# Optimization experiments

Measured on AMD Instinct MI355X. Metric: run time of the kernel, lower is better.

## Reference

```python
import jax, jax.numpy as jnp
import numpy as np

TOP_K = 32
NUM_RBF = 16
D_MIN, D_MAX = 2.0, 22.0
MAX_REL = 32  # max_relative_feature

# atom index order: N=0, Ca=1, C=2, O=3, Cb=4
# 24 (query, neighbor) atom pairs, in the exact order of the torch RBF_all list
_PA = np.array([0,2,3,4,1,1,1,1,0,0,0,4,4,3,0,2,3,4,2,3,4,2,3,2])
_PB = np.array([0,2,3,4,0,2,3,4,2,3,4,2,3,2,1,1,1,1,0,0,0,4,4,3])


def setup_inputs() -> dict:
    key = jax.random.key(0)
    ks = jax.random.split(key, 6)
    B, L = 4, 2048
    X = jax.random.normal(ks[0], (B, L, 4, 3), jnp.float32) * 3.0  # coords, ~protein scale
    mask = jnp.ones((B, L), jnp.float32)
    residue_idx = jnp.tile(jnp.arange(L, dtype=jnp.int32)[None, :], (B, 1))
    chain_labels = jax.random.randint(ks[1], (B, L), 0, 4)
    W_pos = jax.random.normal(ks[2], (2 * MAX_REL + 2, 16), jnp.float32) * 0.1  # [66,16]
    b_pos = jnp.zeros((16,), jnp.float32)
    W_edge = jax.random.normal(ks[3], (16 + 25 * NUM_RBF, 128), jnp.float32) * 0.05  # [416,128]
    ln_gamma = jnp.ones((128,), jnp.float32)
    ln_beta = jnp.zeros((128,), jnp.float32)
    return dict(X=X, mask=mask, residue_idx=residue_idx, chain_labels=chain_labels,
                W_pos=W_pos, b_pos=b_pos, W_edge=W_edge, ln_gamma=ln_gamma, ln_beta=ln_beta)


def _rbf(D):
    mu = jnp.linspace(D_MIN, D_MAX, NUM_RBF)
    sigma = (D_MAX - D_MIN) / NUM_RBF
    return jnp.exp(-(((D[..., None] - mu) / sigma) ** 2))


def reference(X, mask, residue_idx, chain_labels, W_pos, b_pos, W_edge, ln_gamma, ln_beta):
    B, L = X.shape[0], X.shape[1]
    N, Ca, C, O = X[:, :, 0], X[:, :, 1], X[:, :, 2], X[:, :, 3]
    b = Ca - N
    c = C - Ca
    a = jnp.cross(b, c)
    Cb = -0.58273431 * a + 0.56802827 * b - 0.54067466 * c + Ca

    # kNN graph on Ca distances (masked)
    m2 = mask[:, None, :] * mask[:, :, None]                      # [B,L,L]
    dX = Ca[:, None, :, :] - Ca[:, :, None, :]
    D = m2 * jnp.sqrt(jnp.sum(dX * dX, -1) + 1e-6)                # [B,L,L]
    D_max = jnp.max(D, -1, keepdims=True)
    D_adjust = D + (1.0 - m2) * D_max
    neg_vals, E_idx = jax.lax.top_k(-D_adjust, TOP_K)             # smallest-k
    D_neighbors = -neg_vals                                       # [B,L,K]

    atoms = jnp.stack([N, Ca, C, O, Cb], 0)                       # [5,B,L,3]
    bidx = jnp.arange(B)[:, None, None]
    nbr = atoms[:, bidx, E_idx]                                   # [5,B,L,K,3] gathered neighbor coords

    # 24 cross-atom RBFs (gather-then-distance == distance-then-gather)
    Aq = atoms[_PA]                                               # [24,B,L,3]
    Nk = nbr[_PB]                                                 # [24,B,L,K,3]
    Dp = jnp.sqrt(jnp.sum((Aq[:, :, :, None, :] - Nk) ** 2, -1) + 1e-6)  # [24,B,L,K]
    R0 = _rbf(D_neighbors)                                        # [B,L,K,16] (Ca-Ca)
    Rp = jnp.moveaxis(_rbf(Dp), 0, 3).reshape(B, L, TOP_K, 24 * NUM_RBF)
    RBF_all = jnp.concatenate([R0, Rp], -1)                       # [B,L,K,400]

    # positional / chain encodings
    ridx_nbr = residue_idx[bidx, E_idx]                           # [B,L,K]
    offset = residue_idx[:, :, None] - ridx_nbr
    ch_nbr = chain_labels[bidx, E_idx]
    E_chains = (chain_labels[:, :, None] == ch_nbr).astype(jnp.int32)
    d = jnp.clip(offset + MAX_REL, 0, 2 * MAX_REL) * E_chains + (1 - E_chains) * (2 * MAX_REL + 1)
    E_pos = W_pos[d] + b_pos                                      # one-hot @ W == row gather

    E = jnp.concatenate([E_pos, RBF_all], -1) @ W_edge            # [B,L,K,128]
    mu = E.mean(-1, keepdims=True)
    var = E.var(-1, keepdims=True)
    E = (E - mu) / jnp.sqrt(var + 1e-5) * ln_gamma + ln_beta
    return E, E_idx
```

## Files before the change

kernel.cpp:

```cpp
#include <hip/hip_runtime.h>
#include <stdint.h>

typedef _Float16 v8h __attribute__((ext_vector_type(8)));
typedef _Float16 v4h __attribute__((ext_vector_type(4)));
typedef float v4f __attribute__((ext_vector_type(4)));

#define BB 4
#define LL 2048
#define TOPK 32
#define NF 416
#define NOUT 128
#define NBINS 4096
#define NCAND 128
#define FBS 72

__device__ __constant__ int c_PA[24] = {0,2,3,4,1,1,1,1,0,0,0,4,4,3,0,2,3,4,2,3,4,2,3,2};
__device__ __constant__ int c_PB[24] = {0,2,3,4,0,2,3,4,2,3,4,2,3,2,1,1,1,1,0,0,0,4,4,3};

#define OFF_ATOMS 0u
#define OFF_CA    524288u
#define OFF_WT    655360u

#define HPERM(x) ((((x) & 15) << 8) | ((x) >> 4))

static __device__ inline int tk_bin(unsigned u) {
  int v = (int)(u >> 17) - 8000;
  v = v < 0 ? 0 : v;
  return v > 4095 ? 4095 : v;
}

static __device__ inline float dist_np(float4 a, float4 b) {
#pragma clang fp contract(off)
  float dx = a.x - b.x, dy = a.y - b.y, dz = a.z - b.z;
  float s = ((dx * dx + dy * dy) + dz * dz) + 1e-6f;
  return sqrtf(s);
}

static __device__ inline unsigned long long umin64(unsigned long long a, unsigned long long b) {
  return a < b ? a : b;
}
static __device__ inline unsigned long long umax64(unsigned long long a, unsigned long long b) {
  return a > b ? a : b;
}

static __device__ inline void rbf16w(float d, _Float16* dst) {
  v8h z = {};
  *(v8h*)dst = z;
  *(v8h*)(dst + 8) = z;
  float m0f = ceilf((d - 7.204f) * 0.75f);
  m0f = fmaxf(0.0f, fminf(8.0f, m0f));
  const float C  = 0.96089780f;
  const float SC = 1.28119707f;
  float a0 = d * C - 1.92179560f - m0f * SC;
  _Float16* p = dst + (int)m0f;
#pragma unroll
  for (int t = 0; t < 8; ++t) {
    float a = a0 - (float)t * SC;
    float v = __builtin_amdgcn_exp2f(-(a * a));
    p[t] = (_Float16)v;
  }
}

static __device__ inline float pdist(const float* qa, const float* nb, int pp) {
  int ia = c_PA[pp] * 3, ib = c_PB[pp] * 3;
  float dx = qa[ia] - nb[ib];
  float dy = qa[ia + 1] - nb[ib + 1];
  float dz = qa[ia + 2] - nb[ib + 2];
  return sqrtf(dx * dx + dy * dy + dz * dz + 1e-6f);
}

__global__ __launch_bounds__(256) void prep_kernel(const float* __restrict__ X,
                                                   const float* __restrict__ W_edge,
                                                   float4* __restrict__ atomsP,
                                                   float4* __restrict__ CaP,
                                                   _Float16* __restrict__ Wt) {
  int idx = blockIdx.x * 256 + threadIdx.x;
  if (idx < BB * LL) {
    const float* xp = X + (size_t)idx * 12;
    float Nx = xp[0], Ny = xp[1], Nz = xp[2];
    float Cax = xp[3], Cay = xp[4], Caz = xp[5];
    float Cx = xp[6], Cy = xp[7], Cz = xp[8];
    float Ox = xp[9], Oy = xp[10], Oz = xp[11];
    float bx = Cax - Nx, by = Cay - Ny, bz = Caz - Nz;
    float cx = Cx - Cax, cy = Cy - Cay, cz = Cz - Caz;
    float ax = by * cz - bz * cy;
    float ay = bz * cx - bx * cz;
    float az = bx * cy - by * cx;
    float Cbx = -0.58273431f * ax + 0.56802827f * bx - 0.54067466f * cx + Cax;
    float Cby = -0.58273431f * ay + 0.56802827f * by - 0.54067466f * cy + Cay;
    float Cbz = -0.58273431f * az + 0.56802827f * bz - 0.54067466f * cz + Caz;
    atomsP[(size_t)idx * 4 + 0] = make_float4(Nx, Ny, Nz, Cax);
    atomsP[(size_t)idx * 4 + 1] = make_float4(Cay, Caz, Cx, Cy);
    atomsP[(size_t)idx * 4 + 2] = make_float4(Cz, Ox, Oy, Oz);
    atomsP[(size_t)idx * 4 + 3] = make_float4(Cbx, Cby, Cbz, 0.f);
    CaP[idx] = make_float4(Cax, Cay, Caz, 0.f);
  } else {
    int t = idx - BB * LL;
    if (t < NOUT * NF) {
      int n = t / NF;
      int k = t - n * NF;
      Wt[t] = (_Float16)W_edge[(size_t)k * NOUT + n];
    }
  }
}

__global__ __launch_bounds__(256) void topk_kernel(const float4* __restrict__ CaP,
                                                   float* __restrict__ outIdx) {
  __shared__ int hist[NBINS];
  __shared__ unsigned long long cand[NCAND];
  __shared__ int cnt;
  __shared__ int cb_s;
  __shared__ int wtot[4];
  int bid = blockIdx.x;
  int b = bid >> 11;
  int i = bid & (LL - 1);
  int tid = threadIdx.x;
  int lane = tid & 63, wid = tid >> 6;

  {
    int4 z4 = make_int4(0, 0, 0, 0);
    int4* h4 = (int4*)hist;
#pragma unroll
    for (int t = 0; t < NBINS / 1024; ++t) h4[tid + t * 256] = z4;
  }
  if (tid < NCAND) cand[tid] = ~0ull;
  if (tid == 0) cnt = 0;

  const float4* Cb_ = CaP + (size_t)b * LL;
  float4 ci = Cb_[i];
  unsigned long long key[8];
#pragma unroll
  for (int t = 0; t < 8; ++t) {
    int j = tid + (t << 8);
    float d = dist_np(ci, Cb_[j]);
    key[t] = ((unsigned long long)__float_as_uint(d) << 32) | (unsigned)j;
  }
  __syncthreads();
#pragma unroll
  for (int t = 0; t < 8; ++t) {
    atomicAdd(&hist[HPERM(tk_bin((unsigned)(key[t] >> 32)))], 1);
  }
  __syncthreads();

  int base_bin = tid * (NBINS / 256);
  int psum = 0;
#pragma unroll
  for (int t = 0; t < NBINS / 256; ++t) psum += hist[HPERM(base_bin + t)];
  int incl = psum;
#pragma unroll
  for (int off = 1; off < 64; off <<= 1) {
    int o = __shfl_up(incl, off);
    if (lane >= off) incl += o;
  }
  if (lane == 63) wtot[wid] = incl;
  __syncthreads();
  int wbase = 0;
  for (int w = 0; w < wid; ++w) wbase += wtot[w];
  int base = wbase + incl - psum;
  if (base < TOPK && base + psum >= TOPK) {
    int run = base;
    for (int t = 0; t < NBINS / 256; ++t) {
      int h = hist[HPERM(base_bin + t)];
      if (run < TOPK && run + h >= TOPK) { cb_s = base_bin + t; break; }
      run += h;
    }
  }
  __syncthreads();

  int cb = cb_s;
#pragma unroll
  for (int t = 0; t < 8; ++t) {
    if (tk_bin((unsigned)(key[t] >> 32)) <= cb) {
      int slot = atomicAdd(&cnt, 1);
      if (slot < NCAND) cand[slot] = key[t];
    }
  }
  __syncthreads();

  if (wid == 0) {
    int C = cnt;
    unsigned long long x = cand[lane];
    if (C <= 64) {
#pragma unroll
      for (int k = 2; k <= 64; k <<= 1) {
#pragma unroll
        for (int j = k >> 1; j >= 1; j >>= 1) {
          unsigned long long px = __shfl_xor(x, j);
          bool up = ((lane & k) == 0);
          bool low = ((lane & j) == 0);
          x = (low == up) ? umin64(x, px) : umax64(x, px);
        }
      }
    } else {
      unsigned long long y = cand[lane + 64];
#pragma unroll
      for (int k = 2; k <= 128; k <<= 1) {
#pragma unroll
        for (int j = 64; j >= 1; j >>= 1) {
          if (j >= k) continue;
          if (j == 64) {
            unsigned long long mn = umin64(x, y), mx = umax64(x, y);
            x = mn; y = mx;
          } else {
            unsigned long long px = __shfl_xor(x, j);
            bool upx = ((lane & k) == 0);
            bool lowx = ((lane & j) == 0);
            x = (lowx == upx) ? umin64(x, px) : umax64(x, px);
            unsigned long long py = __shfl_xor(y, j);
            bool upy = (((lane + 64) & k) == 0);
            y = (lowx == upy) ? umin64(y, py) : umax64(y, py);
          }
        }
      }
    }
    if (lane < TOPK) {
      int j = (int)(x & 0xffffffffull);
      outIdx[bid * TOPK + lane] = (float)j;
    }
  }
}

__global__ __launch_bounds__(512, 6) void edge_kernel(
    const float4* __restrict__ atomsP, const float4* __restrict__ CaP,
    const _Float16* __restrict__ Wt, const float* __restrict__ outIdxF,
    const int* __restrict__ ridx, const int* __restrict__ chain,
    const float* __restrict__ W_pos, const float* __restrict__ b_pos,
    const float* __restrict__ gamma, const float* __restrict__ beta,
    float* __restrict__ outE) {
  __shared__ __align__(16) _Float16 Fb[2][128][FBS];
  __shared__ float na_f[128][17];
  __shared__ float qa_f[4][16];
  __shared__ float dnbr_s[128];
  __shared__ int dpos_s[128];
  __shared__ int nidx_s[128];
  __shared__ float partS[128][5];
  __shared__ float partQ[128][5];
  __shared__ float2 mr[128];

  int bid = blockIdx.x;
  int b = bid >> 9;
  int tid = threadIdx.x;
  int g0 = bid * 4;

  if (tid < 128) {
    int r = tid >> 5;
    int j = (int)outIdxF[(size_t)bid * 128 + tid];
    nidx_s[tid] = j;
    dnbr_s[tid] = dist_np(CaP[g0 + r], CaP[(size_t)b * LL + j]);
    int ri = ridx[g0 + r], rj = ridx[b * LL + j];
    int off = ri - rj + 32;
    off = off < 0 ? 0 : (off > 64 ? 64 : off);
    dpos_s[tid] = (chain[g0 + r] == chain[b * LL + j]) ? off : 65;
  } else if (tid < 144) {
    int q16 = tid - 128;
    int r = q16 >> 2, q = q16 & 3;
    float4 v = atomsP[(size_t)(g0 + r) * 4 + q];
    qa_f[r][q * 4 + 0] = v.x; qa_f[r][q * 4 + 1] = v.y;
    qa_f[r][q * 4 + 2] = v.z; qa_f[r][q * 4 + 3] = v.w;
  }
  __syncthreads();

  int e = tid >> 2, g = tid & 3;
  int rr = e >> 5;
  {
    float4 v = atomsP[((size_t)b * LL + nidx_s[e]) * 4 + g];
    na_f[e][g * 4 + 0] = v.x; na_f[e][g * 4 + 1] = v.y;
    na_f[e][g * 4 + 2] = v.z; na_f[e][g * 4 + 3] = v.w;
  }

  {
    int dp = dpos_s[e];
    v4h hp;
#pragma unroll
    for (int t = 0; t < 4; ++t)
      hp[t] = (_Float16)(W_pos[dp * 16 + g * 4 + t] + b_pos[g * 4 + t]);
    *(v4h*)&Fb[0][e][g * 4] = hp;
  }
  if (g == 0) {
    rbf16w(dnbr_s[e], &Fb[0][e][16]);
  } else if (g <= 2) {
    int pp = g - 1;
    rbf16w(pdist(qa_f[rr], na_f[e], pp), &Fb[0][e][32 + pp * 16]);
  }
  __syncthreads();

  int lane = tid & 63, wv = tid >> 6;
  int mt = wv & 1, nh = wv >> 1;
  int lm = lane & 15, lq = lane >> 4;
  const _Float16* bp0 = Wt + (size_t)(nh * 32 + lm) * NF + lq * 8;
  const _Float16* bp1 = bp0 + 16 * NF;
  v4f acc[4][2];
#pragma unroll
  for (int t = 0; t < 4; ++t) { acc[t][0] = (v4f){0,0,0,0}; acc[t][1] = (v4f){0,0,0,0}; }

#pragma unroll
  for (int c = 0; c < 7; ++c) {
    if (c < 6) {
      int pp = 4 * c + 2 + g;
      if (pp < 24) {
        float d = pdist(qa_f[rr], na_f[e], pp);
        rbf16w(d, &Fb[(c & 1) ^ 1][e][g * 16]);
      }
    }
    __builtin_amdgcn_s_setprio(1);
#pragma unroll
    for (int kk = 0; kk < 2; ++kk) {
      if (c == 6 && kk == 1) break;
      v8h B0 = *(const v8h*)(bp0 + c * 64 + kk * 32);
      v8h B1 = *(const v8h*)(bp1 + c * 64 + kk * 32);
#pragma unroll
      for (int t = 0; t < 4; ++t) {
        v8h A = *(const v8h*)&Fb[c & 1][mt * 64 + t * 16 + lm][lq * 8 + kk * 32];
        acc[t][0] = __builtin_amdgcn_mfma_f32_16x16x32_f16(A, B0, acc[t][0], 0, 0, 0);
        acc[t][1] = __builtin_amdgcn_mfma_f32_16x16x32_f16(A, B1, acc[t][1], 0, 0, 0);
      }
    }
    __builtin_amdgcn_s_setprio(0);
    if (c < 6) __syncthreads();
  }

#pragma unroll
  for (int t = 0; t < 4; ++t) {
#pragma unroll
    for (int r = 0; r < 4; ++r) {
      float s = acc[t][0][r] + acc[t][1][r];
      float q = acc[t][0][r] * acc[t][0][r] + acc[t][1][r] * acc[t][1][r];
#pragma unroll
      for (int off = 1; off <= 8; off <<= 1) {
        s += __shfl_xor(s, off);
        q += __shfl_xor(q, off);
      }
      if (lm == 0) {
        int row = mt * 64 + t * 16 + lq * 4 + r;
        partS[row][nh] = s;
        partQ[row][nh] = q;
      }
    }
  }
  __syncthreads();
  if (tid < 128) {
    float S = (partS[tid][0] + partS[tid][1]) + (partS[tid][2] + partS[tid][3]);
    float Q = (partQ[tid][0] + partQ[tid][1]) + (partQ[tid][2] + partQ[tid][3]);
    float mean = S * (1.0f / 128.0f);
    float var = Q * (1.0f / 128.0f) - mean * mean;
    mr[tid] = make_float2(mean, 1.0f / sqrtf(var + 1e-5f));
  }
  __syncthreads();
  float gm0 = gamma[nh * 32 + lm], gm1 = gamma[nh * 32 + 16 + lm];
  float bt0 = beta[nh * 32 + lm], bt1 = beta[nh * 32 + 16 + lm];
  float* op = outE + (size_t)bid * 128 * NOUT + nh * 32 + lm;
#pragma unroll
  for (int t = 0; t < 4; ++t) {
#pragma unroll
    for (int r = 0; r < 4; ++r) {
      int row = mt * 64 + t * 16 + lq * 4 + r;
      float2 m = mr[row];
      float* p = op + (size_t)row * NOUT;
      p[0]  = (acc[t][0][r] - m.x) * m.y * gm0 + bt0;
      p[16] = (acc[t][1][r] - m.x) * m.y * gm1 + bt1;
    }
  }
}

extern "C" void kernel_launch(void* const* d_in, const int* in_sizes, int n_in,
                              void* d_out, int out_size, void* d_ws, size_t ws_size,
                              hipStream_t stream) {
  const float* X = (const float*)d_in[0];
  const int* ridx = (const int*)d_in[2];
  const int* chain = (const int*)d_in[3];
  const float* W_pos = (const float*)d_in[4];
  const float* b_pos = (const float*)d_in[5];
  const float* W_edge = (const float*)d_in[6];
  const float* gamma = (const float*)d_in[7];
  const float* beta = (const float*)d_in[8];

  float* outE = (float*)d_out;
  float* outIdx = outE + (size_t)BB * LL * TOPK * NOUT;

  char* ws = (char*)d_ws;
  float4* atomsP = (float4*)(ws + OFF_ATOMS);
  float4* CaP = (float4*)(ws + OFF_CA);
  _Float16* Wt = (_Float16*)(ws + OFF_WT);

  prep_kernel<<<240, 256, 0, stream>>>(X, W_edge, atomsP, CaP, Wt);
  topk_kernel<<<BB * LL, 256, 0, stream>>>(CaP, outIdx);
  edge_kernel<<<BB * LL / 4, 512, 0, stream>>>(atomsP, CaP, Wt, outIdx, ridx, chain,
                                               W_pos, b_pos, gamma, beta, outE);
}
```

Before: 229.6 us.

## Fuse top-k neighbor selection into edge kernel reusing shared memory

Removes the separate topk kernel and runs the histogram-based top-k selection for each of the block's 4 query residues inside the edge kernel, aliasing the histogram and candidate buffers onto the feature and neighbor-atom shared arrays. Neighbor indices and distances stay in shared memory, so the edge kernel no longer reads outIdx back from global memory or recomputes Ca-Ca distances, and one launch is saved. In exchange, each edge block runs four serialized top-k passes with many barriers before its GEMM phase, which may lengthen the critical path per block and lose the parallelism of the 8192 independent topk blocks.

```diff
diff --git a/kernel.cpp b/kernel.cpp
--- a/kernel.cpp
+++ b/kernel.cpp
@@ -104,131 +104,15 @@
   }
 }
 
-__global__ __launch_bounds__(256) void topk_kernel(const float4* __restrict__ CaP,
-                                                   float* __restrict__ outIdx) {
-  __shared__ int hist[NBINS];
-  __shared__ unsigned long long cand[NCAND];
-  __shared__ int cnt;
-  __shared__ int cb_s;
-  __shared__ int wtot[4];
-  int bid = blockIdx.x;
-  int b = bid >> 11;
-  int i = bid & (LL - 1);
-  int tid = threadIdx.x;
-  int lane = tid & 63, wid = tid >> 6;
-
-  {
-    int4 z4 = make_int4(0, 0, 0, 0);
-    int4* h4 = (int4*)hist;
-#pragma unroll
-    for (int t = 0; t < NBINS / 1024; ++t) h4[tid + t * 256] = z4;
-  }
-  if (tid < NCAND) cand[tid] = ~0ull;
-  if (tid == 0) cnt = 0;
-
-  const float4* Cb_ = CaP + (size_t)b * LL;
-  float4 ci = Cb_[i];
-  unsigned long long key[8];
-#pragma unroll
-  for (int t = 0; t < 8; ++t) {
-    int j = tid + (t << 8);
-    float d = dist_np(ci, Cb_[j]);
-    key[t] = ((unsigned long long)__float_as_uint(d) << 32) | (unsigned)j;
-  }
-  __syncthreads();
-#pragma unroll
-  for (int t = 0; t < 8; ++t) {
-    atomicAdd(&hist[HPERM(tk_bin((unsigned)(key[t] >> 32)))], 1);
-  }
-  __syncthreads();
-
-  int base_bin = tid * (NBINS / 256);
-  int psum = 0;
-#pragma unroll
-  for (int t = 0; t < NBINS / 256; ++t) psum += hist[HPERM(base_bin + t)];
-  int incl = psum;
-#pragma unroll
-  for (int off = 1; off < 64; off <<= 1) {
-    int o = __shfl_up(incl, off);
-    if (lane >= off) incl += o;
-  }
-  if (lane == 63) wtot[wid] = incl;
-  __syncthreads();
-  int wbase = 0;
-  for (int w = 0; w < wid; ++w) wbase += wtot[w];
-  int base = wbase + incl - psum;
-  if (base < TOPK && base + psum >= TOPK) {
-    int run = base;
-    for (int t = 0; t < NBINS / 256; ++t) {
-      int h = hist[HPERM(base_bin + t)];
-      if (run < TOPK && run + h >= TOPK) { cb_s = base_bin + t; break; }
-      run += h;
-    }
-  }
-  __syncthreads();
-
-  int cb = cb_s;
-#pragma unroll
-  for (int t = 0; t < 8; ++t) {
-    if (tk_bin((unsigned)(key[t] >> 32)) <= cb) {
-      int slot = atomicAdd(&cnt, 1);
-      if (slot < NCAND) cand[slot] = key[t];
-    }
-  }
-  __syncthreads();
-
-  if (wid == 0) {
-    int C = cnt;
-    unsigned long long x = cand[lane];
-    if (C <= 64) {
-#pragma unroll
-      for (int k = 2; k <= 64; k <<= 1) {
-#pragma unroll
-        for (int j = k >> 1; j >= 1; j >>= 1) {
-          unsigned long long px = __shfl_xor(x, j);
-          bool up = ((lane & k) == 0);
-          bool low = ((lane & j) == 0);
-          x = (low == up) ? umin64(x, px) : umax64(x, px);
-        }
-      }
-    } else {
-      unsigned long long y = cand[lane + 64];
-#pragma unroll
-      for (int k = 2; k <= 128; k <<= 1) {
-#pragma unroll
-        for (int j = 64; j >= 1; j >>= 1) {
-          if (j >= k) continue;
-          if (j == 64) {
-            unsigned long long mn = umin64(x, y), mx = umax64(x, y);
-            x = mn; y = mx;
-          } else {
-            unsigned long long px = __shfl_xor(x, j);
-            bool upx = ((lane & k) == 0);
-            bool lowx = ((lane & j) == 0);
-            x = (lowx == upx) ? umin64(x, px) : umax64(x, px);
-            unsigned long long py = __shfl_xor(y, j);
-            bool upy = (((lane + 64) & k) == 0);
-            y = (lowx == upy) ? umin64(y, py) : umax64(y, py);
-          }
-        }
-      }
-    }
-    if (lane < TOPK) {
-      int j = (int)(x & 0xffffffffull);
-      outIdx[bid * TOPK + lane] = (float)j;
-    }
-  }
-}
-
 __global__ __launch_bounds__(512, 6) void edge_kernel(
     const float4* __restrict__ atomsP, const float4* __restrict__ CaP,
-    const _Float16* __restrict__ Wt, const float* __restrict__ outIdxF,
+    const _Float16* __restrict__ Wt,
     const int* __restrict__ ridx, const int* __restrict__ chain,
     const float* __restrict__ W_pos, const float* __restrict__ b_pos,
     const float* __restrict__ gamma, const float* __restrict__ beta,
-    float* __restrict__ outE) {
+    float* __restrict__ outE, float* __restrict__ outIdx) {
   __shared__ __align__(16) _Float16 Fb[2][128][FBS];
-  __shared__ float na_f[128][17];
+  __shared__ __align__(16) float na_f[128][17];
   __shared__ float qa_f[4][16];
   __shared__ float dnbr_s[128];
   __shared__ int dpos_s[128];
@@ -236,17 +120,128 @@
   __shared__ float partS[128][5];
   __shared__ float partQ[128][5];
   __shared__ float2 mr[128];
+  __shared__ int wtot[8];
+  __shared__ int cnt;
+  __shared__ int cb_s;
+  int* hist = (int*)&Fb[0][0][0];
+  unsigned long long* cand = (unsigned long long*)&na_f[0][0];
 
   int bid = blockIdx.x;
   int b = bid >> 9;
   int tid = threadIdx.x;
   int g0 = bid * 4;
+  int lane = tid & 63, wid = tid >> 6;
+
+  const float4* Cb_ = CaP + (size_t)b * LL;
+
+  for (int r = 0; r < 4; ++r) {
+    {
+      int4 z4 = make_int4(0, 0, 0, 0);
+      ((int4*)hist)[tid] = z4;
+      ((int4*)hist)[tid + 512] = z4;
+    }
+    if (tid < NCAND) cand[tid] = ~0ull;
+    if (tid == 0) cnt = 0;
+
+    float4 ci = CaP[g0 + r];
+    unsigned long long key[4];
+#pragma unroll
+    for (int t = 0; t < 4; ++t) {
+      int j = tid + (t << 9);
+      float d = dist_np(ci, Cb_[j]);
+      key[t] = ((unsigned long long)__float_as_uint(d) << 32) | (unsigned)j;
+    }
+    __syncthreads();
+#pragma unroll
+    for (int t = 0; t < 4; ++t) {
+      atomicAdd(&hist[HPERM(tk_bin((unsigned)(key[t] >> 32)))], 1);
+    }
+    __syncthreads();
+
+    int base_bin = tid * (NBINS / 512);
+    int psum = 0;
+#pragma unroll
+    for (int t = 0; t < NBINS / 512; ++t) psum += hist[HPERM(base_bin + t)];
+    int incl = psum;
+#pragma unroll
+    for (int off = 1; off < 64; off <<= 1) {
+      int o = __shfl_up(incl, off);
+      if (lane >= off) incl += o;
+    }
+    if (lane == 63) wtot[wid] = incl;
+    __syncthreads();
+    int wbase = 0;
+    for (int w = 0; w < wid; ++w) wbase += wtot[w];
+    int base = wbase + incl - psum;
+    if (base < TOPK && base + psum >= TOPK) {
+      int run = base;
+      for (int t = 0; t < NBINS / 512; ++t) {
+        int h = hist[HPERM(base_bin + t)];
+        if (run < TOPK && run + h >= TOPK) { cb_s = base_bin + t; break; }
+        run += h;
+      }
+    }
+    __syncthreads();
+
+    int cb = cb_s;
+#pragma unroll
+    for (int t = 0; t < 4; ++t) {
+      if (tk_bin((unsigned)(key[t] >> 32)) <= cb) {
+        int slot = atomicAdd(&cnt, 1);
+        if (slot < NCAND) cand[slot] = key[t];
+      }
+    }
+    __syncthreads();
+
+    if (wid == 0) {
+      int C = cnt;
+      unsigned long long x = cand[lane];
+      if (C <= 64) {
+#pragma unroll
+        for (int k = 2; k <= 64; k <<= 1) {
+#pragma unroll
+          for (int j = k >> 1; j >= 1; j >>= 1) {
+            unsigned long long px = __shfl_xor(x, j);
+            bool up = ((lane & k) == 0);
+            bool low = ((lane & j) == 0);
+            x = (low == up) ? umin64(x, px) : umax64(x, px);
+          }
+        }
+      } else {
+        unsigned long long y = cand[lane + 64];
+#pragma unroll
+        for (int k = 2; k <= 128; k <<= 1) {
+#pragma unroll
+          for (int j = 64; j >= 1; j >>= 1) {
+            if (j >= k) continue;
+            if (j == 64) {
+              unsigned long long mn = umin64(x, y), mx = umax64(x, y);
+              x = mn; y = mx;
+            } else {
+              unsigned long long px = __shfl_xor(x, j);
+              bool upx = ((lane & k) == 0);
+              bool lowx = ((lane & j) == 0);
+              x = (lowx == upx) ? umin64(x, px) : umax64(x, px);
+              unsigned long long py = __shfl_xor(y, j);
+              bool upy = (((lane + 64) & k) == 0);
+              y = (lowx == upy) ? umin64(y, py) : umax64(y, py);
+            }
+          }
+        }
+      }
+      if (lane < TOPK) {
+        int j = (int)(x & 0xffffffffull);
+        outIdx[(size_t)(g0 + r) * TOPK + lane] = (float)j;
+        nidx_s[r * TOPK + lane] = j;
+        dnbr_s[r * TOPK + lane] = __uint_as_float((unsigned)(x >> 32));
+      }
+    }
+    __syncthreads();
+  }
 
   if (tid < 128) {
     int r = tid >> 5;
-    int j = (int)outIdxF[(size_t)bid * 128 + tid];
-    nidx_s[tid] = j;
-    dnbr_s[tid] = dist_np(CaP[g0 + r], CaP[(size_t)b * LL + j]);
+    int j = nidx_s[tid];
     int ri = ridx[g0 + r], rj = ridx[b * LL + j];
     int off = ri - rj + 32;
     off = off < 0 ? 0 : (off > 64 ? 64 : off);
@@ -284,7 +279,7 @@
   }
   __syncthreads();
 
-  int lane = tid & 63, wv = tid >> 6;
+  int wv = tid >> 6;
   int mt = wv & 1, nh = wv >> 1;
   int lm = lane & 15, lq = lane >> 4;
   const _Float16* bp0 = Wt + (size_t)(nh * 32 + lm) * NF + lq * 8;
@@ -383,7 +378,6 @@
   _Float16* Wt = (_Float16*)(ws + OFF_WT);
 
   prep_kernel<<<240, 256, 0, stream>>>(X, W_edge, atomsP, CaP, Wt);
-  topk_kernel<<<BB * LL, 256, 0, stream>>>(CaP, outIdx);
-  edge_kernel<<<BB * LL / 4, 512, 0, stream>>>(atomsP, CaP, Wt, outIdx, ridx, chain,
-                                               W_pos, b_pos, gamma, beta, outE);
-}
+  edge_kernel<<<BB * LL / 4, 512, 0, stream>>>(atomsP, CaP, Wt, ridx, chain,
+                                               W_pos, b_pos, gamma, beta, outE, outIdx);
+}
```

Measured after the change: 246.5 us. 7.4% more time.

## Assign one wavefront per query row in top-k with a coarser 512-bin histogram

Applied to the files above, without the earlier changes.

The top-k selection kernel now processes four query rows per block, one per 64-lane wavefront, instead of a whole 256-thread block per row. Each wavefront keeps its own 512-bin histogram, candidate buffer and counter, so the block-wide __syncthreads barriers give way to wave-level ballot/shuffle and s_waitcnt lgkmcnt(0) waits. The aim is to cut barrier and histogram-clearing overhead and launch fewer blocks. In exchange each lane computes 32 distances, and the coarser bins can let more candidates land in the boundary bin. If more than 128 candidates arrive, the extras are dropped, which risks wrong neighbours for clustered inputs.

```diff
diff --git a/kernel.cpp b/kernel.cpp
--- a/kernel.cpp
+++ b/kernel.cpp
@@ -10,7 +10,6 @@
 #define TOPK 32
 #define NF 416
 #define NOUT 128
-#define NBINS 4096
 #define NCAND 128
 #define FBS 72
 
@@ -21,12 +20,10 @@
 #define OFF_CA    524288u
 #define OFF_WT    655360u
 
-#define HPERM(x) ((((x) & 15) << 8) | ((x) >> 4))
-
-static __device__ inline int tk_bin(unsigned u) {
-  int v = (int)(u >> 17) - 8000;
+static __device__ inline int wbin(unsigned u) {
+  int v = (int)(u >> 19) - 1870;
   v = v < 0 ? 0 : v;
-  return v > 4095 ? 4095 : v;
+  return v > 511 ? 511 : v;
 }
 
 static __device__ inline float dist_np(float4 a, float4 b) {
@@ -106,117 +103,122 @@
 
 __global__ __launch_bounds__(256) void topk_kernel(const float4* __restrict__ CaP,
                                                    float* __restrict__ outIdx) {
-  __shared__ int hist[NBINS];
-  __shared__ unsigned long long cand[NCAND];
-  __shared__ int cnt;
-  __shared__ int cb_s;
-  __shared__ int wtot[4];
-  int bid = blockIdx.x;
-  int b = bid >> 11;
-  int i = bid & (LL - 1);
+  __shared__ int hist[4][512];
+  __shared__ unsigned long long cand[4][NCAND];
+  __shared__ int cnt[4];
+
   int tid = threadIdx.x;
   int lane = tid & 63, wid = tid >> 6;
+  int q = blockIdx.x * 4 + wid;
+  int b = q >> 11;
+  int i = q & (LL - 1);
+
+  int* h = hist[wid];
+  unsigned long long* cd = cand[wid];
 
   {
-    int4 z4 = make_int4(0, 0, 0, 0);
-    int4* h4 = (int4*)hist;
-#pragma unroll
-    for (int t = 0; t < NBINS / 1024; ++t) h4[tid + t * 256] = z4;
-  }
-  if (tid < NCAND) cand[tid] = ~0ull;
-  if (tid == 0) cnt = 0;
+    int4 z = make_int4(0, 0, 0, 0);
+    ((int4*)h)[lane] = z;
+    ((int4*)h)[lane + 64] = z;
+    cd[lane] = ~0ull;
+    cd[lane + 64] = ~0ull;
+    if (lane == 0) cnt[wid] = 0;
+  }
 
   const float4* Cb_ = CaP + (size_t)b * LL;
   float4 ci = Cb_[i];
-  unsigned long long key[8];
-#pragma unroll
-  for (int t = 0; t < 8; ++t) {
-    int j = tid + (t << 8);
-    float d = dist_np(ci, Cb_[j]);
-    key[t] = ((unsigned long long)__float_as_uint(d) << 32) | (unsigned)j;
-  }
-  __syncthreads();
-#pragma unroll
-  for (int t = 0; t < 8; ++t) {
-    atomicAdd(&hist[HPERM(tk_bin((unsigned)(key[t] >> 32)))], 1);
-  }
-  __syncthreads();
-
-  int base_bin = tid * (NBINS / 256);
+  unsigned db[32];
+#pragma unroll
+  for (int t = 0; t < 32; ++t) {
+    int j = lane + (t << 6);
+    db[t] = __float_as_uint(dist_np(ci, Cb_[j]));
+  }
+  asm volatile("s_waitcnt lgkmcnt(0)" ::: "memory");
+#pragma unroll
+  for (int t = 0; t < 32; ++t) {
+    atomicAdd(&h[wbin(db[t])], 1);
+  }
+  asm volatile("s_waitcnt lgkmcnt(0)" ::: "memory");
+
+  int pb[8];
   int psum = 0;
-#pragma unroll
-  for (int t = 0; t < NBINS / 256; ++t) psum += hist[HPERM(base_bin + t)];
+  {
+    int4 a0 = ((int4*)h)[lane * 2];
+    int4 a1 = ((int4*)h)[lane * 2 + 1];
+    pb[0] = a0.x; pb[1] = a0.y; pb[2] = a0.z; pb[3] = a0.w;
+    pb[4] = a1.x; pb[5] = a1.y; pb[6] = a1.z; pb[7] = a1.w;
+#pragma unroll
+    for (int t = 0; t < 8; ++t) psum += pb[t];
+  }
   int incl = psum;
 #pragma unroll
   for (int off = 1; off < 64; off <<= 1) {
     int o = __shfl_up(incl, off);
     if (lane >= off) incl += o;
   }
-  if (lane == 63) wtot[wid] = incl;
-  __syncthreads();
-  int wbase = 0;
-  for (int w = 0; w < wid; ++w) wbase += wtot[w];
-  int base = wbase + incl - psum;
-  if (base < TOPK && base + psum >= TOPK) {
+  int base = incl - psum;
+  bool cross = (base < TOPK && incl >= TOPK);
+  int cb_local = 511;
+  if (cross) {
     int run = base;
-    for (int t = 0; t < NBINS / 256; ++t) {
-      int h = hist[HPERM(base_bin + t)];
-      if (run < TOPK && run + h >= TOPK) { cb_s = base_bin + t; break; }
-      run += h;
-    }
-  }
-  __syncthreads();
-
-  int cb = cb_s;
-#pragma unroll
-  for (int t = 0; t < 8; ++t) {
-    if (tk_bin((unsigned)(key[t] >> 32)) <= cb) {
-      int slot = atomicAdd(&cnt, 1);
-      if (slot < NCAND) cand[slot] = key[t];
-    }
-  }
-  __syncthreads();
-
-  if (wid == 0) {
-    int C = cnt;
-    unsigned long long x = cand[lane];
-    if (C <= 64) {
-#pragma unroll
-      for (int k = 2; k <= 64; k <<= 1) {
-#pragma unroll
-        for (int j = k >> 1; j >= 1; j >>= 1) {
+#pragma unroll
+    for (int t = 0; t < 8; ++t) {
+      if (run < TOPK && run + pb[t] >= TOPK) { cb_local = lane * 8 + t; break; }
+      run += pb[t];
+    }
+  }
+  unsigned long long cm = __ballot(cross);
+  int src = __ffsll(cm) - 1;
+  int cb = __shfl(cb_local, src);
+
+#pragma unroll
+  for (int t = 0; t < 32; ++t) {
+    if (wbin(db[t]) <= cb) {
+      int slot = atomicAdd(&cnt[wid], 1);
+      if (slot < NCAND)
+        cd[slot] = ((unsigned long long)db[t] << 32) | (unsigned)(lane + (t << 6));
+    }
+  }
+  asm volatile("s_waitcnt lgkmcnt(0)" ::: "memory");
+
+  int C = cnt[wid];
+  unsigned long long x = cd[lane];
+  if (C <= 64) {
+#pragma unroll
+    for (int k = 2; k <= 64; k <<= 1) {
+#pragma unroll
+      for (int j = k >> 1; j >= 1; j >>= 1) {
+        unsigned long long px = __shfl_xor(x, j);
+        bool up = ((lane & k) == 0);
+        bool low = ((lane & j) == 0);
+        x = (low == up) ? umin64(x, px) : umax64(x, px);
+      }
+    }
+  } else {
+    unsigned long long y = cd[lane + 64];
+#pragma unroll
+    for (int k = 2; k <= 128; k <<= 1) {
+#pragma unroll
+      for (int j = 64; j >= 1; j >>= 1) {
+        if (j >= k) continue;
+        if (j == 64) {
+          unsigned long long mn = umin64(x, y), mx = umax64(x, y);
+          x = mn; y = mx;
+        } else {
           unsigned long long px = __shfl_xor(x, j);
-          bool up = ((lane & k) == 0);
-          bool low = ((lane & j) == 0);
-          x = (low == up) ? umin64(x, px) : umax64(x, px);
+          bool upx = ((lane & k) == 0);
+          bool lowx = ((lane & j) == 0);
+          x = (lowx == upx) ? umin64(x, px) : umax64(x, px);
+          unsigned long long py = __shfl_xor(y, j);
+          bool upy = (((lane + 64) & k) == 0);
+          y = (lowx == upy) ? umin64(y, py) : umax64(y, py);
         }
       }
-    } else {
-      unsigned long long y = cand[lane + 64];
-#pragma unroll
-      for (int k = 2; k <= 128; k <<= 1) {
-#pragma unroll
-        for (int j = 64; j >= 1; j >>= 1) {
-          if (j >= k) continue;
-          if (j == 64) {
-            unsigned long long mn = umin64(x, y), mx = umax64(x, y);
-            x = mn; y = mx;
-          } else {
-            unsigned long long px = __shfl_xor(x, j);
-            bool upx = ((lane & k) == 0);
-            bool lowx = ((lane & j) == 0);
-            x = (lowx == upx) ? umin64(x, px) : umax64(x, px);
-            unsigned long long py = __shfl_xor(y, j);
-            bool upy = (((lane + 64) & k) == 0);
-            y = (lowx == upy) ? umin64(y, py) : umax64(y, py);
-          }
-        }
-      }
-    }
-    if (lane < TOPK) {
-      int j = (int)(x & 0xffffffffull);
-      outIdx[bid * TOPK + lane] = (float)j;
-    }
+    }
+  }
+  if (lane < TOPK) {
+    int j = (int)(x & 0xffffffffull);
+    outIdx[(size_t)q * TOPK + lane] = (float)j;
   }
 }
 
@@ -383,7 +385,7 @@
   _Float16* Wt = (_Float16*)(ws + OFF_WT);
 
   prep_kernel<<<240, 256, 0, stream>>>(X, W_edge, atomsP, CaP, Wt);
-  topk_kernel<<<BB * LL, 256, 0, stream>>>(CaP, outIdx);
+  topk_kernel<<<BB * LL / 4, 256, 0, stream>>>(CaP, outIdx);
   edge_kernel<<<BB * LL / 4, 512, 0, stream>>>(atomsP, CaP, Wt, outIdx, ridx, chain,
                                                W_pos, b_pos, gamma, beta, outE);
 }
```

Measured after the change: 222.8 us. 3.0% less time.
